# Kernel tuning notes

Measured on AMD Instinct MI355X. Metric: run time of the kernel, lower is better.

## Reference

```python
import jax, jax.numpy as jnp
import numpy as np

N_NODES = 50000
N_EDGES = 600000
D_IN = 128
D = 128
N_REL = 2
N_LAYERS = 3


def rgcn_conv(h, src, dst, edge_type, weight, root, bias):
    # PyG RGCNConv (no bases), aggr='mean' per relation:
    # out_i = h_i @ root + bias + sum_r mean_{j in N_r(i)} h_j @ W_r
    out = h @ root + bias                      # [N, D]
    hs = h[src]                                # [E, D] gather once
    for r in range(N_REL):
        mask = (edge_type == r).astype(h.dtype)          # [E]
        agg = jax.ops.segment_sum(hs * mask[:, None], dst, num_segments=N_NODES)  # [N, D]
        cnt = jax.ops.segment_sum(mask, dst, num_segments=N_NODES)                # [N]
        mean = agg / jnp.maximum(cnt, 1.0)[:, None]
        out = out + mean @ weight[r]
    return out


def setup_inputs() -> dict:
    key = jax.random.key(0)
    ks = jax.random.split(key, 10)
    x = jax.random.normal(ks[0], (N_NODES, D_IN), dtype=jnp.float32)
    edge_index = jax.random.randint(ks[1], (2, N_EDGES), 0, N_NODES, dtype=jnp.int64)
    edge_attr = jax.random.normal(ks[2], (N_EDGES, N_REL), dtype=jnp.float32)
    # input projection f: Linear(D_IN, D); stored as [D_IN, D] (apply as x @ Wf + bf)
    Wf = jax.random.normal(ks[3], (D_IN, D), dtype=jnp.float32) / np.sqrt(D_IN)
    bf = jnp.zeros((D,), dtype=jnp.float32)
    # per-layer RGCNConv params, stacked over layers
    conv_weight = jax.random.normal(ks[4], (N_LAYERS, N_REL, D, D), dtype=jnp.float32) / np.sqrt(D)
    conv_root = jax.random.normal(ks[5], (N_LAYERS, D, D), dtype=jnp.float32) / np.sqrt(D)
    conv_bias = jnp.zeros((N_LAYERS, D), dtype=jnp.float32)
    return {"x": x, "edge_index": edge_index, "edge_attr": edge_attr,
            "Wf": Wf, "bf": bf, "conv_weight": conv_weight,
            "conv_root": conv_root, "conv_bias": conv_bias}


def reference(x, edge_index, edge_attr, Wf, bf, conv_weight, conv_root, conv_bias):
    src, dst = edge_index[0], edge_index[1]
    edge_type = jnp.argmax(edge_attr, axis=1)           # [E]
    h = jax.nn.relu(x @ Wf + bf)                        # [N, D]
    for l in range(N_LAYERS):
        h = rgcn_conv(h, src, dst, edge_type, conv_weight[l], conv_root[l], conv_bias[l])
        h = jax.nn.relu(h)
    return h
```

## Files before the change

kernel.cpp:

```cpp
#include <hip/hip_runtime.h>
#include <hip/hip_bf16.h>

#define NN 50000
#define NE 600000
#define D 128
#define NREL 2
#define BM 128

typedef __attribute__((ext_vector_type(8))) short bf16x8;
typedef __attribute__((ext_vector_type(4))) float f32x4;

__device__ __forceinline__ float bf2f(short s) {
    return __uint_as_float(((unsigned int)(unsigned short)s) << 16);
}
__device__ __forceinline__ bf16x8 pack_bf8(const float* a) {
    union { bf16x8 v; __hip_bfloat162 h2[4]; } o;
#pragma unroll
    for (int i = 0; i < 4; i++)
        o.h2[i] = __float22bfloat162_rn(make_float2(a[2 * i], a[2 * i + 1]));
    return o.v;
}

#define NEB ((NE + 255) / 256)
#define NWT (16384 + 3 * 49152)
#define NWB ((NWT + 255) / 256)

__global__ void k_pre1(const float* __restrict__ attr,
                       const int* __restrict__ dst,
                       int* __restrict__ cnt,
                       const float* __restrict__ Wf,
                       const float* __restrict__ cw,
                       const float* __restrict__ cr,
                       __hip_bfloat16* __restrict__ wt) {
    if (blockIdx.x < NEB) {
        int i = blockIdx.x * blockDim.x + threadIdx.x;
        if (i >= NE) return;
        float2 a = reinterpret_cast<const float2*>(attr)[i];
        int r = (a.y > a.x) ? 1 : 0;
        atomicAdd(&cnt[dst[i] * 2 + r], 1);
    } else {
        int idx = (blockIdx.x - NEB) * blockDim.x + threadIdx.x;
        if (idx >= NWT) return;
        float v;
        if (idx < 16384) {
            int n = idx >> 7, k = idx & 127;
            v = Wf[k * 128 + n];
        } else {
            int j = idx - 16384;
            int l = j / 49152; j %= 49152;
            int n = j / 384, k = j % 384;
            if (k < 128)      v = cr[((size_t)l * 128 + k) * 128 + n];
            else if (k < 256) v = cw[((size_t)(l * 2 + 0) * 128 + (k - 128)) * 128 + n];
            else              v = cw[((size_t)(l * 2 + 1) * 128 + (k - 256)) * 128 + n];
        }
        wt[idx] = __float2bfloat16(v);
    }
}

__global__ void k_pre2(const int* __restrict__ cnt, float* __restrict__ inv,
                       int* __restrict__ off, int* __restrict__ cur,
                       int* __restrict__ total) {
    int i = blockIdx.x * blockDim.x + threadIdx.x;
    if (i >= NN) return;
    int c0 = cnt[2 * i], c1 = cnt[2 * i + 1];
    inv[2 * i]     = 1.0f / (float)(c0 > 1 ? c0 : 1);
    inv[2 * i + 1] = 1.0f / (float)(c1 > 1 ? c1 : 1);
    int o = atomicAdd(total, c0 + c1);
    off[2 * i] = o;       cur[2 * i] = o;
    off[2 * i + 1] = o + c0; cur[2 * i + 1] = o + c0;
}

__global__ void k_fill(const float* __restrict__ attr,
                       const int* __restrict__ src, const int* __restrict__ dst,
                       int* __restrict__ cursor, int* __restrict__ srcs, int E) {
    int i = blockIdx.x * blockDim.x + threadIdx.x;
    if (i >= E) return;
    float2 a = reinterpret_cast<const float2*>(attr)[i];
    int r = (a.y > a.x) ? 1 : 0;
    int pos = atomicAdd(&cursor[dst[i] * 2 + r], 1);
    srcs[pos] = src[i];
}

__global__ __launch_bounds__(256)
void k_aggregate(const __hip_bfloat16* __restrict__ h,
                 const int* __restrict__ srcs,
                 const int* __restrict__ off, const int* __restrict__ cnt,
                 const float* __restrict__ inv,
                 __hip_bfloat16* __restrict__ agg) {
    int node = (blockIdx.x * blockDim.x + threadIdx.x) >> 6;
    int lane = threadIdx.x & 63;
    if (node >= NN) return;
    int st = off[2 * node];
    int c0 = cnt[2 * node], c01 = c0 + cnt[2 * node + 1];
    int g = lane >> 4, l16 = lane & 15;

    int sv = (lane < c01) ? srcs[st + lane] : 0;

    float acc0[8], acc1[8];
#pragma unroll
    for (int i = 0; i < 8; i++) { acc0[i] = 0.f; acc1[i] = 0.f; }

    if (c01 <= 64) {
        for (int base = 0; base < c01; base += 16) {
            int s[4]; int jj[4];
#pragma unroll
            for (int q = 0; q < 4; q++) {
                jj[q] = base + g + q * 4;
                int t = __shfl(sv, jj[q] & 63);
                s[q] = (jj[q] < c01) ? t : 0;
            }
            bf16x8 v[4];
#pragma unroll
            for (int q = 0; q < 4; q++)
                v[q] = *reinterpret_cast<const bf16x8*>(
                    h + (size_t)s[q] * D + l16 * 8);
#pragma unroll
            for (int q = 0; q < 4; q++) {
                bool ok0 = jj[q] < c0;
                bool ok1 = !ok0 && (jj[q] < c01);
#pragma unroll
                for (int i = 0; i < 8; i++) {
                    float f = bf2f(v[q][i]);
                    acc0[i] += ok0 ? f : 0.f;
                    acc1[i] += ok1 ? f : 0.f;
                }
            }
        }
    } else {
        for (int base = 0; base < c01; base += 16) {
            int s[4]; int jj[4];
#pragma unroll
            for (int q = 0; q < 4; q++) {
                jj[q] = base + g + q * 4;
                int t = __shfl(sv, jj[q] & 63);
                s[q] = (jj[q] < 64) ? t : ((jj[q] < c01) ? srcs[st + jj[q]] : 0);
                if (jj[q] >= c01) s[q] = 0;
            }
            bf16x8 v[4];
#pragma unroll
            for (int q = 0; q < 4; q++)
                v[q] = *reinterpret_cast<const bf16x8*>(
                    h + (size_t)s[q] * D + l16 * 8);
#pragma unroll
            for (int q = 0; q < 4; q++) {
                bool ok0 = jj[q] < c0;
                bool ok1 = !ok0 && (jj[q] < c01);
#pragma unroll
                for (int i = 0; i < 8; i++) {
                    float f = bf2f(v[q][i]);
                    acc0[i] += ok0 ? f : 0.f;
                    acc1[i] += ok1 ? f : 0.f;
                }
            }
        }
    }

#pragma unroll
    for (int i = 0; i < 8; i++) {
        acc0[i] += __shfl_xor(acc0[i], 16);
        acc1[i] += __shfl_xor(acc1[i], 16);
    }
#pragma unroll
    for (int i = 0; i < 8; i++) {
        acc0[i] += __shfl_xor(acc0[i], 32);
        acc1[i] += __shfl_xor(acc1[i], 32);
    }

    if (g == 0) {
        float s0 = inv[2 * node], s1 = inv[2 * node + 1];
        float t0[8], t1[8];
#pragma unroll
        for (int i = 0; i < 8; i++) { t0[i] = acc0[i] * s0; t1[i] = acc1[i] * s1; }
        __hip_bfloat16* dstp = agg + (size_t)node * 256;
        *reinterpret_cast<bf16x8*>(dstp + l16 * 8)       = pack_bf8(t0);
        *reinterpret_cast<bf16x8*>(dstp + 128 + l16 * 8) = pack_bf8(t1);
    }
}

__global__ __launch_bounds__(256)
void k_gemm_proj(const float* __restrict__ X,
                 const __hip_bfloat16* __restrict__ Wt,
                 const float* __restrict__ bias,
                 __hip_bfloat16* __restrict__ out, int N) {
    __shared__ uint4 sB4[1024];
    char* sB = (char*)sB4;
    const int tid = threadIdx.x;
    const int w = tid >> 6;
    const int l16 = tid & 15, lg = (tid & 63) >> 4;

    f32x4 acc[2][8];
#pragma unroll
    for (int m = 0; m < 2; m++)
#pragma unroll
        for (int n = 0; n < 8; n++) acc[m][n] = (f32x4)(0.f);

    const int row0 = blockIdx.x * 128;
#pragma unroll
    for (int kb = 0; kb < 2; ++kb) {
        bf16x8 afr[2][2];
#pragma unroll
        for (int mb = 0; mb < 2; ++mb)
#pragma unroll
            for (int kk = 0; kk < 2; ++kk) {
                int r = row0 + w * 32 + mb * 16 + l16;
                if (r >= N) r = N - 1;
                const float* p = X + (size_t)r * D + kb * 64 + kk * 32 + lg * 8;
                float4 u0 = reinterpret_cast<const float4*>(p)[0];
                float4 u1 = reinterpret_cast<const float4*>(p)[1];
                float t[8] = {u0.x, u0.y, u0.z, u0.w, u1.x, u1.y, u1.z, u1.w};
                afr[mb][kk] = pack_bf8(t);
            }
        __syncthreads();
        {
            int trow = tid >> 3, tb = (tid & 7) * 16;
#pragma unroll
            for (int p = 0; p < 4; ++p) {
                int rr = trow + p * 32;
                uint4 v = *reinterpret_cast<const uint4*>(
                    (const char*)(Wt + (size_t)rr * 128 + kb * 64) + tb);
                *reinterpret_cast<uint4*>(sB + rr * 128 + (tb ^ ((rr & 7) << 4))) = v;
            }
        }
        __syncthreads();
#pragma unroll
        for (int kk = 0; kk < 2; ++kk)
#pragma unroll
            for (int nb = 0; nb < 8; ++nb) {
                int brow = nb * 16 + l16;
                int bcol = kk * 64 + lg * 16;
                bf16x8 bfr = *reinterpret_cast<const bf16x8*>(
                    sB + brow * 128 + (bcol ^ ((brow & 7) << 4)));
                acc[0][nb] = __builtin_amdgcn_mfma_f32_16x16x32_bf16(
                    afr[0][kk], bfr, acc[0][nb], 0, 0, 0);
                acc[1][nb] = __builtin_amdgcn_mfma_f32_16x16x32_bf16(
                    afr[1][kk], bfr, acc[1][nb], 0, 0, 0);
            }
    }
#pragma unroll
    for (int nb = 0; nb < 8; ++nb) {
        int n = nb * 16 + l16;
        float bv = bias[n];
#pragma unroll
        for (int mb = 0; mb < 2; ++mb)
#pragma unroll
            for (int r = 0; r < 4; ++r) {
                int grow = row0 + w * 32 + mb * 16 + lg * 4 + r;
                if (grow < N) {
                    float v = acc[mb][nb][r] + bv;
                    v = v > 0.f ? v : 0.f;
                    out[(size_t)grow * D + n] = __float2bfloat16(v);
                }
            }
    }
}

template <bool OUT_F32>
__global__ __launch_bounds__(256)
void k_gemm_mfma(const __hip_bfloat16* __restrict__ A0, int sA0,
                 const __hip_bfloat16* __restrict__ A1, int sA1,
                 const __hip_bfloat16* __restrict__ A2, int sA2,
                 const __hip_bfloat16* __restrict__ Wt,
                 const float* __restrict__ bias,
                 void* __restrict__ outv, int N) {
    __shared__ uint4 sB4[1024];
    char* sB = (char*)sB4;
    const int tid = threadIdx.x;
    const int w = tid >> 6;
    const int l16 = tid & 15, lg = (tid & 63) >> 4;
    const __hip_bfloat16* As[3] = {A0, A1, A2};
    const int strides[3] = {sA0, sA1, sA2};

    f32x4 acc[2][8];
#pragma unroll
    for (int m = 0; m < 2; m++)
#pragma unroll
        for (int n = 0; n < 8; n++) acc[m][n] = (f32x4)(0.f);

    const size_t row0 = (size_t)blockIdx.x * BM;
#pragma unroll
    for (int kb = 0; kb < 6; ++kb) {
        const __hip_bfloat16* Ac = As[kb >> 1];
        const int strideC = strides[kb >> 1];
        const int koff = (kb & 1) * 64;
        bf16x8 afr[2][2];
#pragma unroll
        for (int mb = 0; mb < 2; ++mb)
#pragma unroll
            for (int kk = 0; kk < 2; ++kk) {
                int r = (int)row0 + w * 32 + mb * 16 + l16;
                if (r >= N) r = N - 1;
                afr[mb][kk] = *reinterpret_cast<const bf16x8*>(
                    Ac + (size_t)r * strideC + koff + kk * 32 + lg * 8);
            }
        __syncthreads();
        {
            int trow = tid >> 3;
            int tb = (tid & 7) * 16;
#pragma unroll
            for (int p = 0; p < 4; ++p) {
                int rr = trow + p * 32;
                uint4 v = *reinterpret_cast<const uint4*>(
                    (const char*)(Wt + (size_t)rr * 384 + kb * 64) + tb);
                *reinterpret_cast<uint4*>(sB + rr * 128 + (tb ^ ((rr & 7) << 4))) = v;
            }
        }
        __syncthreads();
#pragma unroll
        for (int kk = 0; kk < 2; ++kk) {
#pragma unroll
            for (int nb = 0; nb < 8; ++nb) {
                int brow = nb * 16 + l16;
                int bcol = kk * 64 + lg * 16;
                bf16x8 bfr = *reinterpret_cast<const bf16x8*>(
                    sB + brow * 128 + (bcol ^ ((brow & 7) << 4)));
                acc[0][nb] = __builtin_amdgcn_mfma_f32_16x16x32_bf16(
                    afr[0][kk], bfr, acc[0][nb], 0, 0, 0);
                acc[1][nb] = __builtin_amdgcn_mfma_f32_16x16x32_bf16(
                    afr[1][kk], bfr, acc[1][nb], 0, 0, 0);
            }
        }
    }
#pragma unroll
    for (int nb = 0; nb < 8; ++nb) {
        int n = nb * 16 + l16;
        float bv = bias[n];
#pragma unroll
        for (int mb = 0; mb < 2; ++mb) {
#pragma unroll
            for (int r = 0; r < 4; ++r) {
                long grow = (long)row0 + w * 32 + mb * 16 + lg * 4 + r;
                if (grow < N) {
                    float v = acc[mb][nb][r] + bv;
                    v = v > 0.f ? v : 0.f;
                    if (OUT_F32)
                        ((float*)outv)[(size_t)grow * D + n] = v;
                    else
                        ((__hip_bfloat16*)outv)[(size_t)grow * D + n] =
                            __float2bfloat16(v);
                }
            }
        }
    }
}

extern "C" void kernel_launch(void* const* d_in, const int* in_sizes, int n_in,
                              void* d_out, int out_size, void* d_ws, size_t ws_size,
                              hipStream_t stream) {
    const float* x    = (const float*)d_in[0];
    const int*   ei   = (const int*)d_in[1];
    const float* attr = (const float*)d_in[2];
    const float* Wf   = (const float*)d_in[3];
    const float* bf   = (const float*)d_in[4];
    const float* cw   = (const float*)d_in[5];
    const float* cr   = (const float*)d_in[6];
    const float* cb   = (const float*)d_in[7];
    const int* src  = ei;
    const int* dstv = ei + NE;

    char* p = (char*)d_ws;
    __hip_bfloat16* h0   = (__hip_bfloat16*)p; p += (size_t)NN * D * 2;
    __hip_bfloat16* h1   = (__hip_bfloat16*)p; p += (size_t)NN * D * 2;
    __hip_bfloat16* aggb = (__hip_bfloat16*)p; p += (size_t)2 * NN * D * 2;
    __hip_bfloat16* wt   = (__hip_bfloat16*)p; p += (size_t)NWT * 2;
    float* inv  = (float*)p;                p += (size_t)2 * NN * 4;
    int*   cnt  = (int*)p;                  p += (size_t)2 * NN * 4;
    int*   off  = (int*)p;                  p += (size_t)2 * NN * 4;
    int*   cur  = (int*)p;                  p += (size_t)2 * NN * 4;
    int*   srcs = (int*)p;                  p += (size_t)NE * 4;
    int*   total= (int*)p;

    float* outp = (float*)d_out;

    hipMemsetAsync(cnt, 0, (size_t)2 * NN * sizeof(int), stream);
    hipMemsetAsync(total, 0, sizeof(int), stream);
    k_pre1<<<NEB + NWB, 256, 0, stream>>>(attr, dstv, cnt, Wf, cw, cr, wt);
    k_pre2<<<(NN + 255) / 256, 256, 0, stream>>>(cnt, inv, off, cur, total);
    k_fill<<<NEB, 256, 0, stream>>>(attr, src, dstv, cur, srcs, NE);

    k_gemm_proj<<<(NN + 127) / 128, 256, 0, stream>>>(x, wt, bf, h0, NN);

    const int gblocks = (NN + BM - 1) / BM;
    const int ablocks = (NN * 64 + 255) / 256;
    for (int l = 0; l < 3; ++l) {
        const __hip_bfloat16* hin = (l == 1) ? h1 : h0;
        k_aggregate<<<ablocks, 256, 0, stream>>>(hin, srcs, off, cnt, inv, aggb);
        const __hip_bfloat16* wl = wt + 16384 + (size_t)l * 49152;
        const float* bl = cb + (size_t)l * D;
        if (l == 2) {
            k_gemm_mfma<true><<<gblocks, 256, 0, stream>>>(
                hin, 128, aggb, 256, aggb + 128, 256, wl, bl, outp, NN);
        } else {
            __hip_bfloat16* hout = (l == 0) ? h1 : h0;
            k_gemm_mfma<false><<<gblocks, 256, 0, stream>>>(
                hin, 128, aggb, 256, aggb + 128, 256, wl, bl, hout, NN);
        }
    }
}
```

Before: 269.1 us.

## Aggregate four nodes per wavefront with 16-lane groups and packed FMA

The mean-aggregation kernel now assigns four destination nodes to each 64-lane wavefront, one per 16-lane group, instead of one node per wavefront. This removes the cross-group shuffle reductions and the idle lanes that appeared when a node had few neighbours. The mean scaling is folded into per-edge weights that feed packed two-wide float multiply-adds. The loop runs to the largest neighbour count among the four nodes, so lanes in groups with fewer edges sit idle, and each wavefront now has less memory-level parallelism per node.

```diff
diff --git a/kernel.cpp b/kernel.cpp
--- a/kernel.cpp
+++ b/kernel.cpp
@@ -9,6 +9,7 @@
 
 typedef __attribute__((ext_vector_type(8))) short bf16x8;
 typedef __attribute__((ext_vector_type(4))) float f32x4;
+typedef __attribute__((ext_vector_type(2))) float f32x2;
 
 __device__ __forceinline__ float bf2f(short s) {
     return __uint_as_float(((unsigned int)(unsigned short)s) << 16);
@@ -87,94 +88,73 @@
                  const int* __restrict__ off, const int* __restrict__ cnt,
                  const float* __restrict__ inv,
                  __hip_bfloat16* __restrict__ agg) {
-    int node = (blockIdx.x * blockDim.x + threadIdx.x) >> 6;
+    int wid = (blockIdx.x * blockDim.x + threadIdx.x) >> 6;
     int lane = threadIdx.x & 63;
-    if (node >= NN) return;
-    int st = off[2 * node];
-    int c0 = cnt[2 * node], c01 = c0 + cnt[2 * node + 1];
-    int g = lane >> 4, l16 = lane & 15;
-
-    int sv = (lane < c01) ? srcs[st + lane] : 0;
-
-    float acc0[8], acc1[8];
-#pragma unroll
-    for (int i = 0; i < 8; i++) { acc0[i] = 0.f; acc1[i] = 0.f; }
-
-    if (c01 <= 64) {
-        for (int base = 0; base < c01; base += 16) {
-            int s[4]; int jj[4];
-#pragma unroll
-            for (int q = 0; q < 4; q++) {
-                jj[q] = base + g + q * 4;
-                int t = __shfl(sv, jj[q] & 63);
-                s[q] = (jj[q] < c01) ? t : 0;
-            }
-            bf16x8 v[4];
-#pragma unroll
-            for (int q = 0; q < 4; q++)
-                v[q] = *reinterpret_cast<const bf16x8*>(
-                    h + (size_t)s[q] * D + l16 * 8);
-#pragma unroll
-            for (int q = 0; q < 4; q++) {
-                bool ok0 = jj[q] < c0;
-                bool ok1 = !ok0 && (jj[q] < c01);
-#pragma unroll
-                for (int i = 0; i < 8; i++) {
-                    float f = bf2f(v[q][i]);
-                    acc0[i] += ok0 ? f : 0.f;
-                    acc1[i] += ok1 ? f : 0.f;
-                }
-            }
-        }
-    } else {
-        for (int base = 0; base < c01; base += 16) {
-            int s[4]; int jj[4];
-#pragma unroll
-            for (int q = 0; q < 4; q++) {
-                jj[q] = base + g + q * 4;
-                int t = __shfl(sv, jj[q] & 63);
-                s[q] = (jj[q] < 64) ? t : ((jj[q] < c01) ? srcs[st + jj[q]] : 0);
-                if (jj[q] >= c01) s[q] = 0;
-            }
-            bf16x8 v[4];
-#pragma unroll
-            for (int q = 0; q < 4; q++)
-                v[q] = *reinterpret_cast<const bf16x8*>(
-                    h + (size_t)s[q] * D + l16 * 8);
-#pragma unroll
-            for (int q = 0; q < 4; q++) {
-                bool ok0 = jj[q] < c0;
-                bool ok1 = !ok0 && (jj[q] < c01);
-#pragma unroll
-                for (int i = 0; i < 8; i++) {
-                    float f = bf2f(v[q][i]);
-                    acc0[i] += ok0 ? f : 0.f;
-                    acc1[i] += ok1 ? f : 0.f;
-                }
-            }
-        }
-    }
-
-#pragma unroll
-    for (int i = 0; i < 8; i++) {
-        acc0[i] += __shfl_xor(acc0[i], 16);
-        acc1[i] += __shfl_xor(acc1[i], 16);
-    }
-#pragma unroll
-    for (int i = 0; i < 8; i++) {
-        acc0[i] += __shfl_xor(acc0[i], 32);
-        acc1[i] += __shfl_xor(acc1[i], 32);
-    }
-
-    if (g == 0) {
-        float s0 = inv[2 * node], s1 = inv[2 * node + 1];
-        float t0[8], t1[8];
-#pragma unroll
-        for (int i = 0; i < 8; i++) { t0[i] = acc0[i] * s0; t1[i] = acc1[i] * s1; }
-        __hip_bfloat16* dstp = agg + (size_t)node * 256;
-        *reinterpret_cast<bf16x8*>(dstp + l16 * 8)       = pack_bf8(t0);
-        *reinterpret_cast<bf16x8*>(dstp + 128 + l16 * 8) = pack_bf8(t1);
-    }
+    int nb = wid * 4;
+    if (nb >= NN) return;
+    const int g = lane >> 4, l16 = lane & 15;
+    int node = nb + g;
+    bool nv = node < NN;
+    int nn = nv ? node : (NN - 1);
+
+    int st  = off[2 * nn];
+    int c0  = nv ? cnt[2 * nn] : 0;
+    int c01 = c0 + (nv ? cnt[2 * nn + 1] : 0);
+    float i0 = inv[2 * nn], i1 = inv[2 * nn + 1];
+
+    int sv = (l16 < c01) ? srcs[st + l16] : 0;
+
+    int cm = c01;
+    cm = max(cm, __shfl_xor(cm, 16));
+    cm = max(cm, __shfl_xor(cm, 32));
+
+    f32x2 a0[4], a1[4];
+#pragma unroll
+    for (int p = 0; p < 4; p++) { a0[p] = (f32x2)(0.f); a1[p] = (f32x2)(0.f); }
+
+    const char* hb = (const char*)h;
+    for (int j = 0; j < cm; j += 4) {
+        int s[4]; float w0[4], w1[4];
+#pragma unroll
+        for (int q = 0; q < 4; ++q) {
+            int jj = j + q;
+            int t = __shfl(sv, (lane & 48) + (jj & 15));
+            s[q] = t;
+            if (jj >= 16 && jj < c01) s[q] = srcs[st + jj];
+            if (jj >= c01) s[q] = 0;
+            w0[q] = (jj < c0) ? i0 : 0.f;
+            w1[q] = (jj >= c0 && jj < c01) ? i1 : 0.f;
+        }
+        uint4 v[4];
+#pragma unroll
+        for (int q = 0; q < 4; ++q)
+            v[q] = *reinterpret_cast<const uint4*>(
+                hb + (size_t)s[q] * 256 + l16 * 16);
+#pragma unroll
+        for (int q = 0; q < 4; ++q) {
+            f32x2 w0v = {w0[q], w0[q]}, w1v = {w1[q], w1[q]};
+            unsigned uu[4] = {v[q].x, v[q].y, v[q].z, v[q].w};
+#pragma unroll
+            for (int p = 0; p < 4; ++p) {
+                f32x2 val;
+                val.x = __uint_as_float(uu[p] << 16);
+                val.y = __uint_as_float(uu[p] & 0xffff0000u);
+                a0[p] += val * w0v;
+                a1[p] += val * w1v;
+            }
+        }
+    }
+
+    if (!nv) return;
+    float t0[8], t1[8];
+#pragma unroll
+    for (int p = 0; p < 4; p++) {
+        t0[2 * p] = a0[p].x; t0[2 * p + 1] = a0[p].y;
+        t1[2 * p] = a1[p].x; t1[2 * p + 1] = a1[p].y;
+    }
+    __hip_bfloat16* dp = agg + (size_t)node * 256;
+    *reinterpret_cast<bf16x8*>(dp + l16 * 8)       = pack_bf8(t0);
+    *reinterpret_cast<bf16x8*>(dp + 128 + l16 * 8) = pack_bf8(t1);
 }
 
 __global__ __launch_bounds__(256)
@@ -380,7 +360,7 @@
     k_gemm_proj<<<(NN + 127) / 128, 256, 0, stream>>>(x, wt, bf, h0, NN);
 
     const int gblocks = (NN + BM - 1) / BM;
-    const int ablocks = (NN * 64 + 255) / 256;
+    const int ablocks = ((NN + 3) / 4 * 64 + 255) / 256;
     for (int l = 0; l < 3; ++l) {
         const __hip_bfloat16* hin = (l == 1) ? h1 : h0;
         k_aggregate<<<ablocks, 256, 0, stream>>>(hin, srcs, off, cnt, inv, aggb);
```

Result: faster. 230.2 us (-14.5%).
